# Optimization experiments

Measured on AMD Instinct MI355X. Metric: run time of the kernel, lower is better.

## Reference

```python
import jax, jax.numpy as jnp
import numpy as np
from jax import lax

BIG = 1e6  # sentinel 1D distance when no zero seen yet (squared stays finite in fp32)


def edt_2d(binary):
    """Exact Euclidean distance transform of a (B, H, W) binary image.

    Matches scipy.ndimage.distance_transform_edt: for each nonzero pixel,
    distance to the nearest zero pixel. Separable formulation:
      pass 1: g[b,i,c]   = min_r |i - r| s.t. binary[b,r,c] == 0   (two scans)
      pass 2: d2[b,i,j]  = min_c g[b,i,c]^2 + (j - c)^2            (broadcast-min)
    """
    B, H, W = binary.shape
    xs = jnp.moveaxis(binary, 1, 0)  # (H, B, W) -> scan over rows

    def sweep(carry, x):
        d = jnp.where(x == 0, 0.0, carry + 1.0)
        return d, d

    init = jnp.full((B, W), BIG, dtype=binary.dtype)
    _, down = lax.scan(sweep, init, xs)
    _, up = lax.scan(sweep, init, xs, reverse=True)
    g = jnp.moveaxis(jnp.minimum(down, up), 0, 1)  # (B, H, W) vertical 1D EDT

    j = jnp.arange(W, dtype=binary.dtype)
    diff2 = (j[:, None] - j[None, :]) ** 2  # (W_out, W_src)
    # (B, H, 1, W) + (W, W) -> min over source column axis
    d2 = jnp.min(g[:, :, None, :] ** 2 + diff2[None, None, :, :], axis=-1)
    return jnp.sqrt(d2)


def combo_loss(pred, target,
               dice_weight=0.5, bce_weight=0.5, boundary_weight=0.1, focal_weight=0.2,
               smooth=1.0, alpha=1.0, gamma=2.0, inner_boundary_weight=1.0):
    p = jax.nn.sigmoid(pred)

    # Dice
    intersection = jnp.sum(p * target)
    union = jnp.sum(p) + jnp.sum(target)
    dice = 1.0 - (2.0 * intersection + smooth) / (union + smooth)

    # BCEWithLogits (stable)
    bce = jnp.mean(jnp.maximum(pred, 0.0) - pred * target
                   + jnp.log1p(jnp.exp(-jnp.abs(pred))))

    # Boundary loss (torch thresholds raw pred > 0.5, detached -> stop_gradient)
    pred_bin = lax.stop_gradient((pred > 0.5).astype(pred.dtype))[:, 0]    # (B,H,W)
    targ_bin = lax.stop_gradient(target.astype(pred.dtype))[:, 0]          # (B,H,W)
    # per-sample mean then batch mean == global mean (equal-size images)
    boundary = inner_boundary_weight * jnp.mean(
        jnp.abs(edt_2d(pred_bin) - edt_2d(targ_bin)))

    # Focal
    bce_el = -(target * jnp.log(p) + (1.0 - target) * jnp.log(1.0 - p))
    pt = p * target + (1.0 - p) * (1.0 - target)
    focal = jnp.mean(alpha * (1.0 - pt) ** gamma * bce_el)

    return (dice_weight * dice + bce_weight * bce
            + boundary_weight * boundary + focal_weight * focal)


def setup_inputs() -> dict:
    key = jax.random.key(0)
    k1, k2 = jax.random.split(key)
    B, C, H, W = 4, 1, 256, 256
    pred = jax.random.normal(k1, (B, C, H, W), dtype=jnp.float32)
    target = jax.random.bernoulli(k2, 0.5, (B, C, H, W)).astype(jnp.float32)
    return {"pred": pred, "target": target}


def reference(pred, target):
    return combo_loss(pred, target)
```

## Files before the change

kernel.cpp:

```cpp
#include <hip/hip_runtime.h>
#include <math.h>

#define BB 4
#define HH 256
#define WW 256
#define NN (BB*HH*WW)
typedef unsigned long long u64;

#define MASK_OFF_BYTES 256
#define SENT 100000

__global__ __launch_bounds__(256)
void build_masks(const float* __restrict__ pred,
                 const float* __restrict__ targ,
                 float* __restrict__ ws) {
    int t = blockIdx.x * 256 + threadIdx.x;
    if (t < 8) ws[t] = 0.0f;

    int c   = t & 255;
    int w   = (t >> 8) & 3;
    int b   = (t >> 10) & 3;
    int img = t >> 12;

    const float* s = (img ? targ : pred) + b * (HH * WW) + (w * 64) * WW + c;
    u64 m = 0;
    #pragma unroll
    for (int r = 0; r < 64; ++r) {
        float x = s[r * WW];
        m |= ((u64)(x <= 0.5f)) << r;
    }
    u64* maskT = (u64*)((char*)ws + MASK_OFF_BYTES);
    maskT[(((img * BB + b) * WW + c) << 2) + w] = m;
}

__global__ __launch_bounds__(256)
void band_fused(const float* __restrict__ pred,
                const float* __restrict__ targ,
                float* __restrict__ ws) {
    __shared__ float2 G[4][WW];
    __shared__ float red[4][6];

    int blk  = blockIdx.x;
    int b    = blk >> 6;
    int band = blk & 63;
    int i0   = band << 2;
    int wq   = i0 >> 6;
    int o0   = i0 & 63;
    int c    = threadIdx.x;

    const u64* maskT = (const u64*)((const char*)ws + MASK_OFF_BYTES);

    float g2v[2][4];
    #pragma unroll
    for (int img = 0; img < 2; ++img) {
        const u64* mp = maskT + (((img * BB + b) * WW + c) << 2);
        u64 M0 = mp[0], M1 = mp[1], M2 = mp[2], M3 = mp[3];

        int t1 = __ffsll(M1), t2 = __ffsll(M2), t3 = __ffsll(M3);
        int f1 = t1 ? 64 + t1 - 1  : SENT;
        int f2 = t2 ? 128 + t2 - 1 : SENT;
        int f3 = t3 ? 192 + t3 - 1 : SENT;
        int r0 = __ffsll(__brevll(M0));
        int r1 = __ffsll(__brevll(M1));
        int r2 = __ffsll(__brevll(M2));
        int l0 = r0 ? 64 - r0  : -SENT;
        int l1 = r1 ? 128 - r1 : -SENT;
        int l2 = r2 ? 192 - r2 : -SENT;

        int s3 = f3;
        int s2 = min(f2, s3);
        int s1 = min(f1, s2);
        int NF = (wq == 0) ? s1 : (wq == 1) ? s2 : (wq == 2) ? s3 : SENT;
        int q0 = l0;
        int q1 = max(q0, l1);
        int q2 = max(q1, l2);
        int PB = (wq == 0) ? -SENT : (wq == 1) ? q0 : (wq == 2) ? q1 : q2;
        u64 Mq = (wq == 0) ? M0 : (wq == 1) ? M1 : (wq == 2) ? M2 : M3;

        #pragma unroll
        for (int kk = 0; kk < 4; ++kk) {
            int i = i0 + kk, o = o0 + kk;
            u64 sh  = Mq >> o;
            int tn  = __ffsll(sh);
            int n   = tn ? i + tn - 1 : NF;
            u64 shl = Mq << (63 - o);
            int tp  = __ffsll(__brevll(shl));
            int p   = tp ? i - (tp - 1) : PB;
            int g   = min(n - i, i - p);
            g2v[img][kk] = (float)g * (float)g;
        }
    }
    #pragma unroll
    for (int kk = 0; kk < 4; ++kk)
        G[kk][c] = make_float2(g2v[0][kk], g2v[1][kk]);
    __syncthreads();

    int row = threadIdx.x >> 6;
    int j0  = threadIdx.x & 63;
    int i   = i0 + row;

    float d2p[4] = {1e30f, 1e30f, 1e30f, 1e30f};
    float d2t[4] = {1e30f, 1e30f, 1e30f, 1e30f};
    for (int cc = 0; cc < WW; ++cc) {
        float2 g = G[row][cc];
        float fd = (float)(j0 - cc);
        #pragma unroll
        for (int k = 0; k < 4; ++k) {
            float d = fd + (float)(64 * k);
            float q = d * d;
            d2p[k] = fminf(d2p[k], g.x + q);
            d2t[k] = fminf(d2t[k], g.y + q);
        }
    }

    float sPT = 0.0f, sP = 0.0f, sT = 0.0f, sBCE = 0.0f, sFOC = 0.0f, sBND = 0.0f;
    #pragma unroll
    for (int k = 0; k < 4; ++k) {
        int j   = j0 + 64 * k;
        int idx = (b * HH + i) * WW + j;
        float x = pred[idx];
        float t = targ[idx];

        sBND += fabsf(sqrtf(d2p[k]) - sqrtf(d2t[k]));

        float p   = 1.0f / (1.0f + expf(-x));
        float ax  = fabsf(x);
        float l1p = log1pf(expf(-ax));
        float bce_el = fmaxf(x, 0.0f) - x * t + l1p;
        float lsx  = fminf(x, 0.0f) - l1p;
        float lsnx = -fmaxf(x, 0.0f) - l1p;
        float bce_f = -(t * lsx + (1.0f - t) * lsnx);
        float pt = p * t + (1.0f - p) * (1.0f - t);
        float om = 1.0f - pt;

        sPT  += p * t;
        sP   += p;
        sT   += t;
        sBCE += bce_el;
        sFOC += om * om * bce_f;
    }

    float vals[6] = { sPT, sP, sT, sBCE, sFOC, sBND };
    int lane = threadIdx.x & 63;
    int wave = threadIdx.x >> 6;
    #pragma unroll
    for (int k = 0; k < 6; ++k) {
        float v = vals[k];
        #pragma unroll
        for (int off = 32; off > 0; off >>= 1)
            v += __shfl_down(v, off, 64);
        if (lane == 0) red[wave][k] = v;
    }
    __syncthreads();
    if (threadIdx.x < 6) {
        float s = red[0][threadIdx.x] + red[1][threadIdx.x]
                + red[2][threadIdx.x] + red[3][threadIdx.x];
        atomicAdd(&ws[threadIdx.x], s);
    }
}

__global__ void finalize(const float* __restrict__ ws, float* __restrict__ out) {
    float inter = ws[0], sp = ws[1], st = ws[2];
    float bce = ws[3], foc = ws[4], bnd = ws[5];
    float invN = 1.0f / (float)NN;
    float dice = 1.0f - (2.0f * inter + 1.0f) / (sp + st + 1.0f);
    float loss = 0.5f * dice + 0.5f * (bce * invN)
               + 0.1f * (bnd * invN) + 0.2f * (foc * invN);
    out[0] = loss;
}

extern "C" void kernel_launch(void* const* d_in, const int* in_sizes, int n_in,
                              void* d_out, int out_size, void* d_ws, size_t ws_size,
                              hipStream_t stream) {
    const float* pred = (const float*)d_in[0];
    const float* targ = (const float*)d_in[1];
    float* ws = (float*)d_ws;

    build_masks<<<32, 256, 0, stream>>>(pred, targ, ws);
    band_fused<<<BB * 64, 256, 0, stream>>>(pred, targ, ws);
    finalize<<<1, 1, 0, stream>>>(ws, (float*)d_out);
}
```

Before: 77.61 us.

## Use expanding-radius early-exit min scan and fold finalize into last block

The horizontal pass of the distance transform now searches outward from each column by radius and stops once r^2 exceeds every current candidate across the wavefront, instead of scanning all 256 source columns. It also remaps threads so each thread owns one column across the four rows of the band. The separate finalize kernel is removed: a completion counter lets the last block compute the loss, saving one launch. The mask kernel is relaunched with smaller blocks. Early exit relies on the data having nearby zeros, and wavefront divergence may limit the savings.

```diff
diff --git a/kernel.cpp b/kernel.cpp
--- a/kernel.cpp
+++ b/kernel.cpp
@@ -10,12 +10,12 @@
 #define MASK_OFF_BYTES 256
 #define SENT 100000
 
-__global__ __launch_bounds__(256)
+__global__ __launch_bounds__(128)
 void build_masks(const float* __restrict__ pred,
                  const float* __restrict__ targ,
                  float* __restrict__ ws) {
-    int t = blockIdx.x * 256 + threadIdx.x;
-    if (t < 8) ws[t] = 0.0f;
+    int t = blockIdx.x * 128 + threadIdx.x;
+    if (t < 9) ws[t] = 0.0f;
 
     int c   = t & 255;
     int w   = (t >> 8) & 3;
@@ -36,9 +36,11 @@
 __global__ __launch_bounds__(256)
 void band_fused(const float* __restrict__ pred,
                 const float* __restrict__ targ,
-                float* __restrict__ ws) {
+                float* __restrict__ ws,
+                float* __restrict__ out) {
     __shared__ float2 G[4][WW];
     __shared__ float red[4][6];
+    __shared__ int amLast;
 
     int blk  = blockIdx.x;
     int b    = blk >> 6;
@@ -95,29 +97,41 @@
         G[kk][c] = make_float2(g2v[0][kk], g2v[1][kk]);
     __syncthreads();
 
-    int row = threadIdx.x >> 6;
-    int j0  = threadIdx.x & 63;
-    int i   = i0 + row;
-
-    float d2p[4] = {1e30f, 1e30f, 1e30f, 1e30f};
-    float d2t[4] = {1e30f, 1e30f, 1e30f, 1e30f};
-    for (int cc = 0; cc < WW; ++cc) {
-        float2 g = G[row][cc];
-        float fd = (float)(j0 - cc);
-        #pragma unroll
-        for (int k = 0; k < 4; ++k) {
-            float d = fd + (float)(64 * k);
-            float q = d * d;
-            d2p[k] = fminf(d2p[k], g.x + q);
-            d2t[k] = fminf(d2t[k], g.y + q);
+    int j = threadIdx.x;
+    float d2p[4], d2t[4];
+    #pragma unroll
+    for (int k = 0; k < 4; ++k) {
+        float2 g = G[k][j];
+        d2p[k] = g.x; d2t[k] = g.y;
+    }
+    for (int r = 1; r < WW; ++r) {
+        float r2 = (float)(r * r);
+        float dmax = fmaxf(fmaxf(fmaxf(d2p[0], d2p[1]), fmaxf(d2p[2], d2p[3])),
+                           fmaxf(fmaxf(d2t[0], d2t[1]), fmaxf(d2t[2], d2t[3])));
+        if (__all(r2 >= dmax)) break;
+        int lo = j - r, hi = j + r;
+        if (lo >= 0) {
+            #pragma unroll
+            for (int k = 0; k < 4; ++k) {
+                float2 g = G[k][lo];
+                d2p[k] = fminf(d2p[k], g.x + r2);
+                d2t[k] = fminf(d2t[k], g.y + r2);
+            }
         }
+        if (hi < WW) {
+            #pragma unroll
+            for (int k = 0; k < 4; ++k) {
+                float2 g = G[k][hi];
+                d2p[k] = fminf(d2p[k], g.x + r2);
+                d2t[k] = fminf(d2t[k], g.y + r2);
+            }
+        }
     }
 
     float sPT = 0.0f, sP = 0.0f, sT = 0.0f, sBCE = 0.0f, sFOC = 0.0f, sBND = 0.0f;
     #pragma unroll
     for (int k = 0; k < 4; ++k) {
-        int j   = j0 + 64 * k;
-        int idx = (b * HH + i) * WW + j;
+        int idx = (b * HH + (i0 + k)) * WW + j;
         float x = pred[idx];
         float t = targ[idx];
 
@@ -156,17 +170,27 @@
         float s = red[0][threadIdx.x] + red[1][threadIdx.x]
                 + red[2][threadIdx.x] + red[3][threadIdx.x];
         atomicAdd(&ws[threadIdx.x], s);
-    }
-}
-
-__global__ void finalize(const float* __restrict__ ws, float* __restrict__ out) {
-    float inter = ws[0], sp = ws[1], st = ws[2];
-    float bce = ws[3], foc = ws[4], bnd = ws[5];
-    float invN = 1.0f / (float)NN;
-    float dice = 1.0f - (2.0f * inter + 1.0f) / (sp + st + 1.0f);
-    float loss = 0.5f * dice + 0.5f * (bce * invN)
+        __threadfence();
+    }
+    __syncthreads();
+
+    if (threadIdx.x == 0) {
+        unsigned old = atomicAdd((unsigned*)(ws + 6), 1u);
+        amLast = (old == 255u);
+    }
+    __syncthreads();
+    if (amLast && threadIdx.x == 0) {
+        float inter = atomicAdd(&ws[0], 0.0f);
+        float sp    = atomicAdd(&ws[1], 0.0f);
+        float st    = atomicAdd(&ws[2], 0.0f);
+        float bce   = atomicAdd(&ws[3], 0.0f);
+        float foc   = atomicAdd(&ws[4], 0.0f);
+        float bnd   = atomicAdd(&ws[5], 0.0f);
+        float invN = 1.0f / (float)NN;
+        float dice = 1.0f - (2.0f * inter + 1.0f) / (sp + st + 1.0f);
+        out[0] = 0.5f * dice + 0.5f * (bce * invN)
                + 0.1f * (bnd * invN) + 0.2f * (foc * invN);
-    out[0] = loss;
+    }
 }
 
 extern "C" void kernel_launch(void* const* d_in, const int* in_sizes, int n_in,
@@ -176,7 +200,6 @@
     const float* targ = (const float*)d_in[1];
     float* ws = (float*)d_ws;
 
-    build_masks<<<32, 256, 0, stream>>>(pred, targ, ws);
-    band_fused<<<BB * 64, 256, 0, stream>>>(pred, targ, ws);
-    finalize<<<1, 1, 0, stream>>>(ws, (float*)d_out);
+    build_masks<<<64, 128, 0, stream>>>(pred, targ, ws);
+    band_fused<<<BB * 64, 256, 0, stream>>>(pred, targ, ws, (float*)d_out);
 }
```

Result: faster. 70.15 us (-9.6%).
